# Optimization experiments

Hardware: AMD Instinct MI355X
Metric: run time of the kernel (lower is better)

## Reference

```python
import jax, jax.numpy as jnp
import numpy as np

B, T, F, H, L = 512, 512, 64, 128, 3


def setup_inputs() -> dict:
    key = jax.random.key(0)
    ks = jax.random.split(key, 6)
    s_in = 1.0 / np.sqrt(F)
    s_h = 1.0 / np.sqrt(H)
    return {
        "x": jax.random.normal(ks[0], (B, T, F), dtype=jnp.float32),
        "Wx0": jax.random.normal(ks[1], (F, 3 * H), dtype=jnp.float32) * s_in,
        "Wx_rest": jax.random.normal(ks[2], (L - 1, H, 3 * H), dtype=jnp.float32) * s_h,
        "Wh": jax.random.normal(ks[3], (L, H, 3 * H), dtype=jnp.float32) * s_h,
        "b": jnp.zeros((L, 3 * H), dtype=jnp.float32),
        "Wd": jax.random.normal(ks[4], (H, H), dtype=jnp.float32) * s_h,
        "bd": jnp.zeros((H,), dtype=jnp.float32),
    }


def _gru_layer(x_seq, Wx, Wh_l, b_l):
    """x_seq: [T, B, Din] -> [T, B, H]. Classic GRU (reset_after=False)."""
    # Precompute input projections for all timesteps in one GEMM: [T, B, 3H]
    gx = jnp.einsum("tbd,dg->tbg", x_seq, Wx) + b_l

    def step(h, gx_t):
        gh = h @ Wh_l                      # [B, 3H]
        xz, xr, xn = jnp.split(gx_t, 3, axis=-1)
        hz, hr, hn = jnp.split(gh, 3, axis=-1)
        z = jax.nn.sigmoid(xz + hz)
        r = jax.nn.sigmoid(xr + hr)
        n = jnp.tanh(xn + r * hn)
        h_new = z * h + (1.0 - z) * n
        return h_new, h_new

    h0 = jnp.zeros((x_seq.shape[1], Wh_l.shape[0]), dtype=x_seq.dtype)
    _, hs = jax.lax.scan(step, h0, gx)
    return hs                              # [T, B, H]


def reference(x, Wx0, Wx_rest, Wh, b, Wd, bd):
    h = jnp.swapaxes(x, 0, 1)              # [T, B, F] time-major for scan
    h = _gru_layer(h, Wx0, Wh[0], b[0])
    for l in range(1, L):                  # small fixed layer loop
        h = _gru_layer(h, Wx_rest[l - 1], Wh[l], b[l])
    h = jnp.swapaxes(h, 0, 1)              # [B, T, H]
    return jax.nn.sigmoid(jnp.einsum("bth,hk->btk", h, Wd) + bd)
```

## Files before the change

### kernel.cpp

```cpp
#include <hip/hip_runtime.h>

namespace {

constexpr int Bb = 512, Tt = 512, Ff = 64, Hh = 128, Gg = 384;
constexpr int CH = 64;
constexpr int NCH = Tt / CH;

using short8  = __attribute__((ext_vector_type(8))) short;
using short4v = __attribute__((ext_vector_type(4))) short;
using f32x4   = __attribute__((ext_vector_type(4))) float;

__device__ __forceinline__ short f2bf(float f) {
  unsigned u = __float_as_uint(f);
  u += 0x7FFFu + ((u >> 16) & 1u);
  return (short)(u >> 16);
}
__device__ __forceinline__ float bf2f(short s) {
  return __uint_as_float(((unsigned)(unsigned short)s) << 16);
}
__device__ __forceinline__ float sigm(float x) { return 1.0f / (1.0f + __expf(-x)); }
__device__ __forceinline__ float tanh_fast(float x) { return 1.0f - 2.0f / (1.0f + __expf(2.0f * x)); }

__device__ __forceinline__ void gl_lds16(const char* g, char* l) {
  __builtin_amdgcn_global_load_lds((const __attribute__((address_space(1))) void*)g,
                                   (__attribute__((address_space(3))) void*)l, 16, 0, 0);
}

__global__ __launch_bounds__(512, 4) void prep(const float* __restrict__ Wx0,
                                               const float* __restrict__ Wxr,
                                               const float* __restrict__ Wh,
                                               const float* __restrict__ Wd,
                                               char* __restrict__ WhF,
                                               char* __restrict__ WxF,
                                               char* __restrict__ WdF) {
  const int id = blockIdx.x * 512 + threadIdx.x;
  const int lane = id & 63, lr = lane & 15, lk = lane >> 4;
  const int q = id >> 6;
  const float* src; int col, ldn, row0; char* dst;
  if (q < 288) {
    const int l = q / 96, rem = q % 96, w = rem / 12, f = rem % 12;
    const int g = f >> 2, ks = f & 3;
    src = Wh + (size_t)l * Hh * Gg; ldn = Gg;
    col = g * 128 + w * 16 + lr; row0 = ks * 32 + lk * 8;
    dst = WhF + (size_t)(q * 64 + lane) * 16;
  } else if (q < 528) {
    int p = q - 288; int base;
    if (p < 48)       { src = Wx0; base = 0; }
    else if (p < 144) { src = Wxr; base = 48; p -= 48; }
    else              { src = Wxr + (size_t)Hh * Gg; base = 144; p -= 144; }
    int ct, ks;
    if (base == 0) { ct = p >> 1; ks = p & 1; } else { ct = p >> 2; ks = p & 3; }
    ldn = Gg; col = ct * 16 + lr; row0 = ks * 32 + lk * 8;
    dst = WxF + (size_t)((base + p) * 64 + lane) * 16;
  } else {
    const int p = q - 528;
    const int ct = p >> 2, ks = p & 3;
    src = Wd; ldn = Hh; col = ct * 16 + lr; row0 = ks * 32 + lk * 8;
    dst = WdF + (size_t)(p * 64 + lane) * 16;
  }
  short8 v;
#pragma unroll
  for (int j = 0; j < 8; ++j) v[j] = f2bf(src[(size_t)(row0 + j) * ldn + col]);
  *(short8*)dst = v;
}

template <int KS>
__device__ void gemm_chunk(const void* __restrict__ src, int t0,
                           const char* __restrict__ wxf,
                           const float* __restrict__ bias,
                           char* __restrict__ gx, int wg, char* at) {
  constexpr int ROWB = KS * 64;
  const int tid = threadIdx.x;
  const int w = tid >> 6, lane = tid & 63, lr = lane & 15, lk = lane >> 4;
  const int trel = wg >> 3, b0 = (wg & 7) * 64;

  if constexpr (KS == 2) {
    const float* x = (const float*)src;
    const int row = tid >> 3, seg = tid & 7;
    const float* pr = x + ((size_t)(b0 + row) * Tt + t0 + trel) * Ff + seg * 8;
    f32x4 a = *(const f32x4*)pr, c = *(const f32x4*)(pr + 4);
    short8 o;
#pragma unroll
    for (int j = 0; j < 4; ++j) { o[j] = f2bf(a[j]); o[4 + j] = f2bf(c[j]); }
    *(short8*)(at + row * ROWB + ((seg * 16) ^ ((row & 7) << 4))) = o;
  } else {
    const char* h = (const char*)src + ((size_t)trel * 512 + b0) * ROWB;
    gl_lds16(h + tid * 16, at + tid * 16);
    gl_lds16(h + 8192 + tid * 16, at + 8192 + tid * 16);
    asm volatile("s_waitcnt vmcnt(0)");
  }
  __syncthreads();

  short8 bw[3][KS];
  float bs[3];
#pragma unroll
  for (int c = 0; c < 3; ++c) {
    const int ct = w * 3 + c;
    bs[c] = bias[ct * 16 + lr];
#pragma unroll
    for (int ks = 0; ks < KS; ++ks)
      bw[c][ks] = *(const short8*)(wxf + (size_t)((ct * KS + ks) * 64 + lane) * 16);
  }

#pragma unroll
  for (int rt = 0; rt < 4; ++rt) {
    const int row = rt * 16 + lr;
    short8 aa[KS];
#pragma unroll
    for (int ks = 0; ks < KS; ++ks)
      aa[ks] = *(const short8*)(at + row * ROWB + ((ks * 64 + lk * 16) ^ ((row & 7) << 4)));
#pragma unroll
    for (int c = 0; c < 3; ++c) {
      f32x4 acc = {0.f, 0.f, 0.f, 0.f};
#pragma unroll
      for (int ks = 0; ks < KS; ++ks)
        acc = __builtin_amdgcn_mfma_f32_16x16x32_bf16(aa[ks], bw[c][ks], acc, 0, 0, 0);
      const int ct = w * 3 + c, sw = ct & 7, g = ct >> 3;
      short4v o;
#pragma unroll
      for (int i = 0; i < 4; ++i) o[i] = f2bf(acc[i] + bs[c]);
      const int rb = (b0 >> 4) + rt;
      *(short4v*)(gx + (size_t)((trel * 32 + rb) * 8 + sw) * 1536 + lane * 24 + g * 8) = o;
    }
  }
}

template <bool DENSE>
__device__ void scan_chunk(const char* __restrict__ gx,
                           const char* __restrict__ whf,
                           short* __restrict__ hstream,
                           float* __restrict__ state, int t0,
                           const char* __restrict__ wdf,
                           const float* __restrict__ bd,
                           float* __restrict__ out, int rb,
                           char* h_buf, float* ob) {
  const int tid = threadIdx.x;
  const int w = tid >> 6, lane = tid & 63, lr = lane & 15, lk = lane >> 4;
  const int col = w * 16 + lr;

  short8 bwh[3][4];
#pragma unroll
  for (int g = 0; g < 3; ++g)
#pragma unroll
    for (int ks = 0; ks < 4; ++ks)
      bwh[g][ks] = *(const short8*)(whf + (size_t)((w * 12 + g * 4 + ks) * 64 + lane) * 16);

  short8 bwd[4]; float bdv = 0.f;
  if constexpr (DENSE) {
#pragma unroll
    for (int ks = 0; ks < 4; ++ks)
      bwd[ks] = *(const short8*)(wdf + (size_t)((w * 4 + ks) * 64 + lane) * 16);
    bdv = bd[col];
  }

  float hreg[4];
  if (t0 == 0) {
#pragma unroll
    for (int i = 0; i < 4; ++i) hreg[i] = 0.f;
    short* hz = (short*)h_buf;
    for (int i = tid; i < 2048; i += 512) hz[i] = 0;
  } else {
    f32x4 s = *(const f32x4*)(state + (size_t)(rb * 512 + tid) * 4);
#pragma unroll
    for (int i = 0; i < 4; ++i) {
      hreg[i] = s[i];
      const int hrow = lk * 4 + i;
      *(short*)(h_buf + hrow * 256 + ((col * 2) ^ ((hrow & 7) << 4))) = f2bf(s[i]);
    }
  }

  auto issue = [&](int trel, short4v* d) {
    const char* p = gx + (size_t)((trel * 32 + rb) * 8 + w) * 1536 + lane * 24;
    d[0] = *(const short4v*)p;
    d[1] = *(const short4v*)(p + 8);
    d[2] = *(const short4v*)(p + 16);
  };
  short4v pfA[3], pfB[3];
  issue(0, pfA);
  issue(1, pfB);
  __syncthreads();

  auto step = [&](int t, short4v* cur) {
    const int pp = t & 1;
    char* const hsrc = h_buf + pp * 4096;
    char* const hdst = h_buf + (1 - pp) * 4096;

    const short4v g0 = cur[0], g1 = cur[1], g2 = cur[2];

    short8 ah[4];
#pragma unroll
    for (int ks = 0; ks < 4; ++ks)
      ah[ks] = *(const short8*)(hsrc + lr * 256 + ((ks * 64 + lk * 16) ^ ((lr & 7) << 4)));

    f32x4 aZ = {0.f, 0.f, 0.f, 0.f}, aR = aZ, aHn = aZ;
#pragma unroll
    for (int ks = 0; ks < 4; ++ks) {
      aZ  = __builtin_amdgcn_mfma_f32_16x16x32_bf16(ah[ks], bwh[0][ks], aZ, 0, 0, 0);
      aR  = __builtin_amdgcn_mfma_f32_16x16x32_bf16(ah[ks], bwh[1][ks], aR, 0, 0, 0);
      aHn = __builtin_amdgcn_mfma_f32_16x16x32_bf16(ah[ks], bwh[2][ks], aHn, 0, 0, 0);
    }
    if (t + 2 < t0 + CH) issue(t + 2 - t0, cur);

    if constexpr (DENSE) {
      if (t > 0) {
        f32x4 aD = {0.f, 0.f, 0.f, 0.f};
#pragma unroll
        for (int ks = 0; ks < 4; ++ks)
          aD = __builtin_amdgcn_mfma_f32_16x16x32_bf16(ah[ks], bwd[ks], aD, 0, 0, 0);
#pragma unroll
        for (int i = 0; i < 4; ++i)
          ob[pp * 2048 + (lk * 4 + i) * 128 + col] = sigm(aD[i] + bdv);
      }
    }

#pragma unroll
    for (int i = 0; i < 4; ++i) {
      const float z = sigm(aZ[i] + bf2f(g0[i]));
      const float r = sigm(aR[i] + bf2f(g1[i]));
      const float n = tanh_fast(bf2f(g2[i]) + r * aHn[i]);
      const float h = z * hreg[i] + (1.f - z) * n;
      hreg[i] = h;
      const int hrow = lk * 4 + i;
      *(short*)(hdst + hrow * 256 + ((col * 2) ^ ((hrow & 7) << 4))) = f2bf(h);
    }

    __builtin_amdgcn_sched_barrier(0);
    asm volatile("s_waitcnt lgkmcnt(0)");
    __builtin_amdgcn_s_barrier();
    __builtin_amdgcn_sched_barrier(0);

    if constexpr (DENSE) {
      if (t > 0) {
        f32x4 v = *(const f32x4*)(ob + pp * 2048 + tid * 4);
        *(f32x4*)(out + ((size_t)(rb * 16 + (tid >> 5)) * Tt + (t - 1)) * Hh + (tid & 31) * 4) = v;
      }
    } else {
      short4v hv = *(const short4v*)(hdst + tid * 8);
      *(short4v*)(hstream + (size_t)((t - t0) * 512 + rb * 16 + (tid >> 5)) * 128 + (tid & 31) * 4) = hv;
    }
  };

  for (int tb = t0; tb < t0 + CH; tb += 2) {
    step(tb, pfA);
    step(tb + 1, pfB);
  }

  {
    f32x4 sv;
#pragma unroll
    for (int i = 0; i < 4; ++i) sv[i] = hreg[i];
    *(f32x4*)(state + (size_t)(rb * 512 + tid) * 4) = sv;
  }

  if constexpr (DENSE) {
    if (t0 + CH == Tt) {
      short8 ah[4];
#pragma unroll
      for (int ks = 0; ks < 4; ++ks)
        ah[ks] = *(const short8*)(h_buf + lr * 256 + ((ks * 64 + lk * 16) ^ ((lr & 7) << 4)));
      f32x4 aD = {0.f, 0.f, 0.f, 0.f};
#pragma unroll
      for (int ks = 0; ks < 4; ++ks)
        aD = __builtin_amdgcn_mfma_f32_16x16x32_bf16(ah[ks], bwd[ks], aD, 0, 0, 0);
#pragma unroll
      for (int i = 0; i < 4; ++i)
        out[((size_t)(rb * 16 + lk * 4 + i) * Tt + (Tt - 1)) * Hh + col] = sigm(aD[i] + bdv);
    }
  }
}

struct GArgs { const void* src; char* gx; const char* wxf; const float* bias; int t0; int isx; };
struct SArgs { const char* gx; short* hstream; float* state; const char* whf; int t0; int dense; };

__global__ __launch_bounds__(512, 1) void gemm_multi(GArgs a0, GArgs a1, GArgs a2) {
  __shared__ char at[16384];
  const int g = blockIdx.x >> 9;
  const int wg = blockIdx.x & 511;
  GArgs a = (g == 0) ? a0 : (g == 1 ? a1 : a2);
  if (a.isx) gemm_chunk<2>(a.src, a.t0, a.wxf, a.bias, a.gx, wg, at);
  else       gemm_chunk<4>(a.src, a.t0, a.wxf, a.bias, a.gx, wg, at);
}

__global__ __launch_bounds__(512, 1) void scan_multi(SArgs a0, SArgs a1, SArgs a2,
                                                     const char* __restrict__ wdf,
                                                     const float* __restrict__ bd,
                                                     float* __restrict__ out) {
  __shared__ char hb[8192];
  __shared__ float ob[4096];
  const int g = blockIdx.x >> 5;
  const int rb = blockIdx.x & 31;
  SArgs a = (g == 0) ? a0 : (g == 1 ? a1 : a2);
  if (a.dense) scan_chunk<true >(a.gx, a.whf, a.hstream, a.state, a.t0, wdf, bd, out, rb, hb, ob);
  else         scan_chunk<false>(a.gx, a.whf, a.hstream, a.state, a.t0, wdf, bd, out, rb, hb, ob);
}

}

extern "C" void kernel_launch(void* const* d_in, const int* in_sizes, int n_in,
                              void* d_out, int out_size, void* d_ws, size_t ws_size,
                              hipStream_t stream) {
  const float* x   = (const float*)d_in[0];
  const float* Wx0 = (const float*)d_in[1];
  const float* Wxr = (const float*)d_in[2];
  const float* Wh  = (const float*)d_in[3];
  const float* b   = (const float*)d_in[4];
  const float* Wd  = (const float*)d_in[5];
  const float* bd  = (const float*)d_in[6];
  float* out = (float*)d_out;

  char* ws = (char*)d_ws;
  char*  WhF   = ws;
  char*  WxF   = ws + 294912;
  char*  WdF   = ws + 540672;
  float* state0 = (float*)(ws + 573440);
  float* state1 = state0 + 65536;
  float* state2 = state1 + 65536;
  char*  gx0 = ws + 2097152;
  char*  gx1 = gx0 + 25165824;
  char*  gx2 = gx1 + 25165824;
  char*  hc  = ws + 2097152 + 3 * 25165824;

  prep<<<70, 512, 0, stream>>>(Wx0, Wxr, Wh, Wd, WhF, WxF, WdF);

  const size_t WXOFF[3] = {0, 49152, 147456};
  for (int r = 0; r < NCH + 2; ++r) {
    GArgs ga[3]; SArgs sa[3]; int n = 0;
    for (int l = 0; l < 3; ++l) {
      const int k = r - l;
      if (k < 0 || k >= NCH) continue;
      const void* src = (l == 0) ? (const void*)x
                                 : (const void*)(hc + ((size_t)((l - 1) * 2 + (k & 1))) * 8388608);
      char*  gxl = (l == 0) ? gx0 : (l == 1 ? gx1 : gx2);
      float* st  = (l == 0) ? state0 : (l == 1 ? state1 : state2);
      ga[n] = { src, gxl, WxF + WXOFF[l], b + l * Gg, k * CH, l == 0 };
      sa[n] = { gxl, (l < 2) ? (short*)(hc + (size_t)(l * 2 + (k & 1)) * 8388608) : (short*)nullptr,
                st, WhF + (size_t)l * 98304, k * CH, l == 2 };
      ++n;
    }
    for (int i = n; i < 3; ++i) { ga[i] = ga[0]; sa[i] = sa[0]; }
    gemm_multi<<<n * 512, 512, 0, stream>>>(ga[0], ga[1], ga[2]);
    scan_multi<<<n * 32, 512, 0, stream>>>(sa[0], sa[1], sa[2], WdF, bd, out);
  }
}
```

Baseline: 1.175 ms.

## Fuse per-chunk input GEMM into scan kernel and fold activation scales into weights

```diff
diff --git a/kernel.cpp b/kernel.cpp
--- a/kernel.cpp
+++ b/kernel.cpp
@@ -3,8 +3,9 @@
 namespace {
 
 constexpr int Bb = 512, Tt = 512, Ff = 64, Hh = 128, Gg = 384;
-constexpr int CH = 64;
-constexpr int NCH = Tt / CH;
+constexpr int CH = 64, NCH = Tt / CH;
+constexpr float SZ = -1.44269504f;
+constexpr float SN =  2.88539008f;
 
 using short8  = __attribute__((ext_vector_type(8))) short;
 using short4v = __attribute__((ext_vector_type(4))) short;
@@ -17,13 +18,6 @@
 }
 __device__ __forceinline__ float bf2f(short s) {
   return __uint_as_float(((unsigned)(unsigned short)s) << 16);
-}
-__device__ __forceinline__ float sigm(float x) { return 1.0f / (1.0f + __expf(-x)); }
-__device__ __forceinline__ float tanh_fast(float x) { return 1.0f - 2.0f / (1.0f + __expf(2.0f * x)); }
-
-__device__ __forceinline__ void gl_lds16(const char* g, char* l) {
-  __builtin_amdgcn_global_load_lds((const __attribute__((address_space(1))) void*)g,
-                                   (__attribute__((address_space(3))) void*)l, 16, 0, 0);
 }
 
 __global__ __launch_bounds__(512, 4) void prep(const float* __restrict__ Wx0,
@@ -36,13 +30,14 @@
   const int id = blockIdx.x * 512 + threadIdx.x;
   const int lane = id & 63, lr = lane & 15, lk = lane >> 4;
   const int q = id >> 6;
-  const float* src; int col, ldn, row0; char* dst;
+  const float* src; int col, ldn, row0; char* dst; float sc;
   if (q < 288) {
     const int l = q / 96, rem = q % 96, w = rem / 12, f = rem % 12;
     const int g = f >> 2, ks = f & 3;
     src = Wh + (size_t)l * Hh * Gg; ldn = Gg;
     col = g * 128 + w * 16 + lr; row0 = ks * 32 + lk * 8;
     dst = WhF + (size_t)(q * 64 + lane) * 16;
+    sc = (g < 2) ? SZ : SN;
   } else if (q < 528) {
     int p = q - 288; int base;
     if (p < 48)       { src = Wx0; base = 0; }
@@ -52,88 +47,80 @@
     if (base == 0) { ct = p >> 1; ks = p & 1; } else { ct = p >> 2; ks = p & 3; }
     ldn = Gg; col = ct * 16 + lr; row0 = ks * 32 + lk * 8;
     dst = WxF + (size_t)((base + p) * 64 + lane) * 16;
+    sc = (ct < 16) ? SZ : SN;
   } else {
     const int p = q - 528;
     const int ct = p >> 2, ks = p & 3;
     src = Wd; ldn = Hh; col = ct * 16 + lr; row0 = ks * 32 + lk * 8;
     dst = WdF + (size_t)(p * 64 + lane) * 16;
+    sc = SZ;
   }
   short8 v;
 #pragma unroll
-  for (int j = 0; j < 8; ++j) v[j] = f2bf(src[(size_t)(row0 + j) * ldn + col]);
+  for (int j = 0; j < 8; ++j) v[j] = f2bf(src[(size_t)(row0 + j) * ldn + col] * sc);
   *(short8*)dst = v;
 }
 
 template <int KS>
-__device__ void gemm_chunk(const void* __restrict__ src, int t0,
+__device__ void gemm_phase(const void* __restrict__ src, int t0,
                            const char* __restrict__ wxf,
                            const float* __restrict__ bias,
-                           char* __restrict__ gx, int wg, char* at) {
-  constexpr int ROWB = KS * 64;
-  const int tid = threadIdx.x;
-  const int w = tid >> 6, lane = tid & 63, lr = lane & 15, lk = lane >> 4;
-  const int trel = wg >> 3, b0 = (wg & 7) * 64;
-
-  if constexpr (KS == 2) {
-    const float* x = (const float*)src;
-    const int row = tid >> 3, seg = tid & 7;
-    const float* pr = x + ((size_t)(b0 + row) * Tt + t0 + trel) * Ff + seg * 8;
-    f32x4 a = *(const f32x4*)pr, c = *(const f32x4*)(pr + 4);
-    short8 o;
-#pragma unroll
-    for (int j = 0; j < 4; ++j) { o[j] = f2bf(a[j]); o[4 + j] = f2bf(c[j]); }
-    *(short8*)(at + row * ROWB + ((seg * 16) ^ ((row & 7) << 4))) = o;
-  } else {
-    const char* h = (const char*)src + ((size_t)trel * 512 + b0) * ROWB;
-    gl_lds16(h + tid * 16, at + tid * 16);
-    gl_lds16(h + 8192 + tid * 16, at + 8192 + tid * 16);
-    asm volatile("s_waitcnt vmcnt(0)");
-  }
-  __syncthreads();
-
+                           char* __restrict__ gx,
+                           int rb, int w, int lane, int lr, int lk) {
   short8 bw[3][KS];
   float bs[3];
 #pragma unroll
   for (int c = 0; c < 3; ++c) {
     const int ct = w * 3 + c;
-    bs[c] = bias[ct * 16 + lr];
+    bs[c] = bias[ct * 16 + lr] * (ct < 16 ? SZ : SN);
 #pragma unroll
     for (int ks = 0; ks < KS; ++ks)
       bw[c][ks] = *(const short8*)(wxf + (size_t)((ct * KS + ks) * 64 + lane) * 16);
   }
-
-#pragma unroll
-  for (int rt = 0; rt < 4; ++rt) {
-    const int row = rt * 16 + lr;
-    short8 aa[KS];
-#pragma unroll
-    for (int ks = 0; ks < KS; ++ks)
-      aa[ks] = *(const short8*)(at + row * ROWB + ((ks * 64 + lk * 16) ^ ((row & 7) << 4)));
+#pragma unroll 2
+  for (int t = 0; t < CH; ++t) {
+    short8 af[KS];
+    if constexpr (KS == 2) {
+      const float* xr = (const float*)src;
+#pragma unroll
+      for (int ks = 0; ks < 2; ++ks) {
+        const float* p = xr + ((size_t)(rb * 16 + lr) * Tt + t0 + t) * Ff + ks * 32 + lk * 8;
+        f32x4 u0 = *(const f32x4*)p, u1 = *(const f32x4*)(p + 4);
+        short8 v;
+#pragma unroll
+        for (int j = 0; j < 4; ++j) { v[j] = f2bf(u0[j]); v[4 + j] = f2bf(u1[j]); }
+        af[ks] = v;
+      }
+    } else {
+      const char* hr = (const char*)src;
+#pragma unroll
+      for (int ks = 0; ks < 4; ++ks)
+        af[ks] = *(const short8*)(hr + ((size_t)t * 512 + rb * 16 + lr) * 256 +
+                                  ((ks * 64 + lk * 16) ^ ((lr & 7) << 4)));
+    }
 #pragma unroll
     for (int c = 0; c < 3; ++c) {
       f32x4 acc = {0.f, 0.f, 0.f, 0.f};
 #pragma unroll
       for (int ks = 0; ks < KS; ++ks)
-        acc = __builtin_amdgcn_mfma_f32_16x16x32_bf16(aa[ks], bw[c][ks], acc, 0, 0, 0);
-      const int ct = w * 3 + c, sw = ct & 7, g = ct >> 3;
+        acc = __builtin_amdgcn_mfma_f32_16x16x32_bf16(af[ks], bw[c][ks], acc, 0, 0, 0);
+      const int ct = w * 3 + c;
       short4v o;
 #pragma unroll
       for (int i = 0; i < 4; ++i) o[i] = f2bf(acc[i] + bs[c]);
-      const int rb = (b0 >> 4) + rt;
-      *(short4v*)(gx + (size_t)((trel * 32 + rb) * 8 + sw) * 1536 + lane * 24 + g * 8) = o;
-    }
-  }
-}
-
-template <bool DENSE>
-__device__ void scan_chunk(const char* __restrict__ gx,
+      *(short4v*)(gx + (size_t)((t * 32 + rb) * 8 + (ct & 7)) * 1536 + lane * 24 + (ct >> 3) * 8) = o;
+    }
+  }
+}
+
+__device__ void scan_phase(const char* __restrict__ gx,
                            const char* __restrict__ whf,
                            short* __restrict__ hstream,
-                           float* __restrict__ state, int t0,
+                           float* __restrict__ state, int t0, int dense,
                            const char* __restrict__ wdf,
-                           const float* __restrict__ bd,
-                           float* __restrict__ out, int rb,
-                           char* h_buf, float* ob) {
+                           const float* __restrict__ bdp,
+                           float* __restrict__ out,
+                           int rb, char* hb, float* ob) {
   const int tid = threadIdx.x;
   const int w = tid >> 6, lane = tid & 63, lr = lane & 15, lk = lane >> 4;
   const int col = w * 16 + lr;
@@ -146,46 +133,47 @@
       bwh[g][ks] = *(const short8*)(whf + (size_t)((w * 12 + g * 4 + ks) * 64 + lane) * 16);
 
   short8 bwd[4]; float bdv = 0.f;
-  if constexpr (DENSE) {
+  if (dense) {
 #pragma unroll
     for (int ks = 0; ks < 4; ++ks)
       bwd[ks] = *(const short8*)(wdf + (size_t)((w * 4 + ks) * 64 + lane) * 16);
-    bdv = bd[col];
+    bdv = bdp[col] * SZ;
+  }
+
+  int hoffs[4];
+#pragma unroll
+  for (int i = 0; i < 4; ++i) {
+    const int row = lk * 4 + i;
+    hoffs[i] = row * 256 + ((col * 2) ^ ((row & 7) << 4));
   }
 
   float hreg[4];
   if (t0 == 0) {
 #pragma unroll
     for (int i = 0; i < 4; ++i) hreg[i] = 0.f;
-    short* hz = (short*)h_buf;
+    short* hz = (short*)hb;
     for (int i = tid; i < 2048; i += 512) hz[i] = 0;
   } else {
     f32x4 s = *(const f32x4*)(state + (size_t)(rb * 512 + tid) * 4);
 #pragma unroll
     for (int i = 0; i < 4; ++i) {
       hreg[i] = s[i];
-      const int hrow = lk * 4 + i;
-      *(short*)(h_buf + hrow * 256 + ((col * 2) ^ ((hrow & 7) << 4))) = f2bf(s[i]);
-    }
-  }
-
-  auto issue = [&](int trel, short4v* d) {
-    const char* p = gx + (size_t)((trel * 32 + rb) * 8 + w) * 1536 + lane * 24;
-    d[0] = *(const short4v*)p;
-    d[1] = *(const short4v*)(p + 8);
-    d[2] = *(const short4v*)(p + 16);
-  };
-  short4v pfA[3], pfB[3];
-  issue(0, pfA);
-  issue(1, pfB);
+      *(short*)(hb + hoffs[i]) = f2bf(s[i]);
+    }
+  }
+
+  const char* gp = gx + (size_t)(rb * 8 + w) * 1536 + lane * 24;
+  short4v pf0[3], pf1[3], pf2[3], pf3[3];
+#pragma unroll
+  for (int j = 0; j < 3; ++j) pf0[j] = *(const short4v*)(gp + j * 8);
+#pragma unroll
+  for (int j = 0; j < 3; ++j) pf1[j] = *(const short4v*)(gp + 393216 + j * 8);
   __syncthreads();
 
-  auto step = [&](int t, short4v* cur) {
+  auto STEP = [&](int t, short4v (&use)[3], short4v (&fill)[3]) {
     const int pp = t & 1;
-    char* const hsrc = h_buf + pp * 4096;
-    char* const hdst = h_buf + (1 - pp) * 4096;
-
-    const short4v g0 = cur[0], g1 = cur[1], g2 = cur[2];
+    char* const hsrc = hb + pp * 4096;
+    char* const hdst = hb + (1 - pp) * 4096;
 
     short8 ah[4];
 #pragma unroll
@@ -199,50 +187,66 @@
       aR  = __builtin_amdgcn_mfma_f32_16x16x32_bf16(ah[ks], bwh[1][ks], aR, 0, 0, 0);
       aHn = __builtin_amdgcn_mfma_f32_16x16x32_bf16(ah[ks], bwh[2][ks], aHn, 0, 0, 0);
     }
-    if (t + 2 < t0 + CH) issue(t + 2 - t0, cur);
-
-    if constexpr (DENSE) {
-      if (t > 0) {
-        f32x4 aD = {0.f, 0.f, 0.f, 0.f};
-#pragma unroll
-        for (int ks = 0; ks < 4; ++ks)
-          aD = __builtin_amdgcn_mfma_f32_16x16x32_bf16(ah[ks], bwd[ks], aD, 0, 0, 0);
-#pragma unroll
-        for (int i = 0; i < 4; ++i)
-          ob[pp * 2048 + (lk * 4 + i) * 128 + col] = sigm(aD[i] + bdv);
-      }
-    }
-
+    if (t + 2 < CH) {
+      const char* p = gp + (size_t)(t + 2) * 393216;
+      fill[0] = *(const short4v*)p;
+      fill[1] = *(const short4v*)(p + 8);
+      fill[2] = *(const short4v*)(p + 16);
+    }
+    const int tg = t0 + t;
+    if (dense && tg > 0) {
+      f32x4 aD = {0.f, 0.f, 0.f, 0.f};
+#pragma unroll
+      for (int ks = 0; ks < 4; ++ks)
+        aD = __builtin_amdgcn_mfma_f32_16x16x32_bf16(ah[ks], bwd[ks], aD, 0, 0, 0);
+#pragma unroll
+      for (int i = 0; i < 4; ++i)
+        ob[pp * 2048 + (lk * 4 + i) * 128 + col] =
+            __builtin_amdgcn_rcpf(1.f + __builtin_amdgcn_exp2f(aD[i] + bdv));
+    }
+
+    float hn4[4];
 #pragma unroll
     for (int i = 0; i < 4; ++i) {
-      const float z = sigm(aZ[i] + bf2f(g0[i]));
-      const float r = sigm(aR[i] + bf2f(g1[i]));
-      const float n = tanh_fast(bf2f(g2[i]) + r * aHn[i]);
-      const float h = z * hreg[i] + (1.f - z) * n;
-      hreg[i] = h;
-      const int hrow = lk * 4 + i;
-      *(short*)(hdst + hrow * 256 + ((col * 2) ^ ((hrow & 7) << 4))) = f2bf(h);
-    }
+      const float gz = bf2f(use[0][i]);
+      const float gr = bf2f(use[1][i]);
+      const float gn = bf2f(use[2][i]);
+      const float z  = __builtin_amdgcn_rcpf(1.f + __builtin_amdgcn_exp2f(aZ[i] + gz));
+      const float rr = __builtin_amdgcn_rcpf(1.f + __builtin_amdgcn_exp2f(aR[i] + gr));
+      const float eu = __builtin_amdgcn_exp2f(__builtin_fmaf(rr, aHn[i], gn));
+      const float nn = __builtin_fmaf(-2.f, __builtin_amdgcn_rcpf(1.f + eu), 1.f);
+      const float h  = __builtin_fmaf(z, hreg[i] - nn, nn);
+      hn4[i] = h; hreg[i] = h;
+    }
+    unsigned p01, p23;
+    asm("v_cvt_pk_bf16_f32 %0, %1, %2" : "=v"(p01) : "v"(hn4[0]), "v"(hn4[1]));
+    asm("v_cvt_pk_bf16_f32 %0, %1, %2" : "=v"(p23) : "v"(hn4[2]), "v"(hn4[3]));
+    *(short*)(hdst + hoffs[0]) = (short)(p01 & 0xffffu);
+    *(short*)(hdst + hoffs[1]) = (short)(p01 >> 16);
+    *(short*)(hdst + hoffs[2]) = (short)(p23 & 0xffffu);
+    *(short*)(hdst + hoffs[3]) = (short)(p23 >> 16);
 
     __builtin_amdgcn_sched_barrier(0);
     asm volatile("s_waitcnt lgkmcnt(0)");
     __builtin_amdgcn_s_barrier();
     __builtin_amdgcn_sched_barrier(0);
 
-    if constexpr (DENSE) {
-      if (t > 0) {
+    if (dense) {
+      if (tg > 0) {
         f32x4 v = *(const f32x4*)(ob + pp * 2048 + tid * 4);
-        *(f32x4*)(out + ((size_t)(rb * 16 + (tid >> 5)) * Tt + (t - 1)) * Hh + (tid & 31) * 4) = v;
+        *(f32x4*)(out + ((size_t)(rb * 16 + (tid >> 5)) * Tt + (tg - 1)) * Hh + (tid & 31) * 4) = v;
       }
     } else {
       short4v hv = *(const short4v*)(hdst + tid * 8);
-      *(short4v*)(hstream + (size_t)((t - t0) * 512 + rb * 16 + (tid >> 5)) * 128 + (tid & 31) * 4) = hv;
+      *(short4v*)(hstream + ((size_t)t * 512 + rb * 16 + (tid >> 5)) * 128 + (tid & 31) * 4) = hv;
     }
   };
 
-  for (int tb = t0; tb < t0 + CH; tb += 2) {
-    step(tb, pfA);
-    step(tb + 1, pfB);
+  for (int tb = 0; tb < CH; tb += 4) {
+    STEP(tb + 0, pf0, pf2);
+    STEP(tb + 1, pf1, pf3);
+    STEP(tb + 2, pf2, pf0);
+    STEP(tb + 3, pf3, pf1);
   }
 
   {
@@ -252,46 +256,48 @@
     *(f32x4*)(state + (size_t)(rb * 512 + tid) * 4) = sv;
   }
 
-  if constexpr (DENSE) {
-    if (t0 + CH == Tt) {
-      short8 ah[4];
-#pragma unroll
-      for (int ks = 0; ks < 4; ++ks)
-        ah[ks] = *(const short8*)(h_buf + lr * 256 + ((ks * 64 + lk * 16) ^ ((lr & 7) << 4)));
-      f32x4 aD = {0.f, 0.f, 0.f, 0.f};
-#pragma unroll
-      for (int ks = 0; ks < 4; ++ks)
-        aD = __builtin_amdgcn_mfma_f32_16x16x32_bf16(ah[ks], bwd[ks], aD, 0, 0, 0);
-#pragma unroll
-      for (int i = 0; i < 4; ++i)
-        out[((size_t)(rb * 16 + lk * 4 + i) * Tt + (Tt - 1)) * Hh + col] = sigm(aD[i] + bdv);
-    }
-  }
-}
-
-struct GArgs { const void* src; char* gx; const char* wxf; const float* bias; int t0; int isx; };
-struct SArgs { const char* gx; short* hstream; float* state; const char* whf; int t0; int dense; };
-
-__global__ __launch_bounds__(512, 1) void gemm_multi(GArgs a0, GArgs a1, GArgs a2) {
-  __shared__ char at[16384];
-  const int g = blockIdx.x >> 9;
-  const int wg = blockIdx.x & 511;
-  GArgs a = (g == 0) ? a0 : (g == 1 ? a1 : a2);
-  if (a.isx) gemm_chunk<2>(a.src, a.t0, a.wxf, a.bias, a.gx, wg, at);
-  else       gemm_chunk<4>(a.src, a.t0, a.wxf, a.bias, a.gx, wg, at);
-}
-
-__global__ __launch_bounds__(512, 1) void scan_multi(SArgs a0, SArgs a1, SArgs a2,
-                                                     const char* __restrict__ wdf,
-                                                     const float* __restrict__ bd,
-                                                     float* __restrict__ out) {
-  __shared__ char hb[8192];
+  if (dense && t0 + CH == Tt) {
+    short8 ah[4];
+#pragma unroll
+    for (int ks = 0; ks < 4; ++ks)
+      ah[ks] = *(const short8*)(hb + lr * 256 + ((ks * 64 + lk * 16) ^ ((lr & 7) << 4)));
+    f32x4 aD = {0.f, 0.f, 0.f, 0.f};
+#pragma unroll
+    for (int ks = 0; ks < 4; ++ks)
+      aD = __builtin_amdgcn_mfma_f32_16x16x32_bf16(ah[ks], bwd[ks], aD, 0, 0, 0);
+#pragma unroll
+    for (int i = 0; i < 4; ++i)
+      out[((size_t)(rb * 16 + lk * 4 + i) * Tt + (Tt - 1)) * Hh + col] =
+          __builtin_amdgcn_rcpf(1.f + __builtin_amdgcn_exp2f(aD[i] + bdv));
+  }
+}
+
+struct LArgs {
+  const void* src; const char* wxf; const char* whf; const float* bias;
+  char* gx; short* hstream; float* state; int t0; int ksx; int dense;
+};
+
+__global__ __launch_bounds__(512, 1) void fused(LArgs a0, LArgs a1, LArgs a2,
+                                                const char* __restrict__ wdf,
+                                                const float* __restrict__ bd,
+                                                float* __restrict__ out) {
+  __shared__ char  hb[8192];
   __shared__ float ob[4096];
   const int g = blockIdx.x >> 5;
   const int rb = blockIdx.x & 31;
-  SArgs a = (g == 0) ? a0 : (g == 1 ? a1 : a2);
-  if (a.dense) scan_chunk<true >(a.gx, a.whf, a.hstream, a.state, a.t0, wdf, bd, out, rb, hb, ob);
-  else         scan_chunk<false>(a.gx, a.whf, a.hstream, a.state, a.t0, wdf, bd, out, rb, hb, ob);
+  LArgs a = (g == 0) ? a0 : (g == 1 ? a1 : a2);
+  const int tid = threadIdx.x;
+  const int w = tid >> 6, lane = tid & 63, lr = lane & 15, lk = lane >> 4;
+
+  if (a.ksx == 2) gemm_phase<2>(a.src, a.t0, a.wxf, a.bias, a.gx, rb, w, lane, lr, lk);
+  else            gemm_phase<4>(a.src, a.t0, a.wxf, a.bias, a.gx, rb, w, lane, lr, lk);
+
+  __builtin_amdgcn_sched_barrier(0);
+  asm volatile("s_waitcnt vmcnt(0)");
+  __builtin_amdgcn_s_barrier();
+  __builtin_amdgcn_sched_barrier(0);
+
+  scan_phase(a.gx, a.whf, a.hstream, a.state, a.t0, a.dense, wdf, bd, out, rb, hb, ob);
 }
 
 }
@@ -309,36 +315,37 @@
   float* out = (float*)d_out;
 
   char* ws = (char*)d_ws;
-  char*  WhF   = ws;
-  char*  WxF   = ws + 294912;
-  char*  WdF   = ws + 540672;
+  char*  WhF    = ws;
+  char*  WxF    = ws + 294912;
+  char*  WdF    = ws + 540672;
   float* state0 = (float*)(ws + 573440);
-  float* state1 = state0 + 65536;
-  float* state2 = state1 + 65536;
-  char*  gx0 = ws + 2097152;
-  char*  gx1 = gx0 + 25165824;
-  char*  gx2 = gx1 + 25165824;
-  char*  hc  = ws + 2097152 + 3 * 25165824;
+  char*  gx0    = ws + 1441792;
+  char*  gx1    = gx0 + 25165824;
+  char*  gx2    = gx1 + 25165824;
+  short* hc     = (short*)(ws + 76939264);
 
   prep<<<70, 512, 0, stream>>>(Wx0, Wxr, Wh, Wd, WhF, WxF, WdF);
 
   const size_t WXOFF[3] = {0, 49152, 147456};
   for (int r = 0; r < NCH + 2; ++r) {
-    GArgs ga[3]; SArgs sa[3]; int n = 0;
+    LArgs la[3]; int n = 0;
     for (int l = 0; l < 3; ++l) {
       const int k = r - l;
       if (k < 0 || k >= NCH) continue;
-      const void* src = (l == 0) ? (const void*)x
-                                 : (const void*)(hc + ((size_t)((l - 1) * 2 + (k & 1))) * 8388608);
-      char*  gxl = (l == 0) ? gx0 : (l == 1 ? gx1 : gx2);
-      float* st  = (l == 0) ? state0 : (l == 1 ? state1 : state2);
-      ga[n] = { src, gxl, WxF + WXOFF[l], b + l * Gg, k * CH, l == 0 };
-      sa[n] = { gxl, (l < 2) ? (short*)(hc + (size_t)(l * 2 + (k & 1)) * 8388608) : (short*)nullptr,
-                st, WhF + (size_t)l * 98304, k * CH, l == 2 };
-      ++n;
-    }
-    for (int i = n; i < 3; ++i) { ga[i] = ga[0]; sa[i] = sa[0]; }
-    gemm_multi<<<n * 512, 512, 0, stream>>>(ga[0], ga[1], ga[2]);
-    scan_multi<<<n * 32, 512, 0, stream>>>(sa[0], sa[1], sa[2], WdF, bd, out);
-  }
-}
+      LArgs& A = la[n++];
+      A.src = (l == 0) ? (const void*)x
+                       : (const void*)(hc + (size_t)((l - 1) * 2 + (k & 1)) * 4194304);
+      A.wxf = WxF + WXOFF[l];
+      A.whf = WhF + (size_t)l * 98304;
+      A.bias = b + l * Gg;
+      A.gx = (l == 0) ? gx0 : (l == 1 ? gx1 : gx2);
+      A.hstream = (l < 2) ? hc + (size_t)(l * 2 + (k & 1)) * 4194304 : nullptr;
+      A.state = state0 + l * 65536;
+      A.t0 = k * CH;
+      A.ksx = (l == 0) ? 2 : 4;
+      A.dense = (l == 2) ? 1 : 0;
+    }
+    for (int i = n; i < 3; ++i) la[i] = la[0];
+    fused<<<n * 32, 512, 0, stream>>>(la[0], la[1], la[2], WdF, bd, out);
+  }
+}
```

New measurement: 1.193 ms. No clear change (+1.6%).
